# Optimization experiments

Hardware: AMD Instinct MI355X
Metric: run time of the kernel (lower is better)

Reference implementation:

```python
import jax, jax.numpy as jnp
import numpy as np

B, T, EMB, H = 8, 1024, 128, 8


def setup_inputs() -> dict:
    key = jax.random.key(0)
    ks = jax.random.split(key, 7)
    s = 0.02
    return {
        "x": jax.random.normal(ks[0], (B, T, EMB), dtype=jnp.float32),
        "mask": jax.random.randint(ks[1], (1, T, T), 0, 2, dtype=jnp.int32),
        "Wk": (jax.random.normal(ks[2], (EMB * H, EMB), dtype=jnp.float32) * s),
        "Wq": (jax.random.normal(ks[3], (EMB * H, EMB), dtype=jnp.float32) * s),
        "Wv": (jax.random.normal(ks[4], (EMB * H, EMB), dtype=jnp.float32) * s),
        "Wu": (jax.random.normal(ks[5], (EMB, EMB * H), dtype=jnp.float32) * s),
        "bu": (jax.random.normal(ks[6], (EMB,), dtype=jnp.float32) * s),
    }


def reference(x, mask, Wk, Wq, Wv, Wu, bu):
    b, t, e = x.shape  # e == emb; per-head dim also == emb in this module
    h = Wk.shape[0] // e
    # projections: (b,t,e) @ (e, h*e) -> (b,t,h,e) -> (b,h,t,e)
    q = (x @ Wq.T).reshape(b, t, h, e).transpose(0, 2, 1, 3)
    k = (x @ Wk.T).reshape(b, t, h, e).transpose(0, 2, 1, 3)
    v = (x @ Wv.T).reshape(b, t, h, e).transpose(0, 2, 1, 3)
    scale = e ** 0.25  # torch scales q and k each by e**(1/4)
    dot = jnp.einsum('bhqe,bhke->bhqk', q / scale, k / scale)
    # causal mask: strictly-upper triangle (offset=1) set to -inf FIRST
    causal = jnp.triu(jnp.ones((t, t), dtype=bool), k=1)
    dot = jnp.where(causal, -jnp.inf, dot)
    # padding mask: where mask==0 set to -1e9 (overwrites -inf where overlapping)
    dot = jnp.where(mask[:, None] == 0, jnp.float32(-1e9), dot)
    attn = jax.nn.softmax(dot, axis=-1)
    out = jnp.einsum('bhqk,bhke->bhqe', attn, v)
    out = out.transpose(0, 2, 1, 3).reshape(b, t, h * e)
    return out @ Wu.T + bu
```

## Files before the change

kernel.cpp:

```cpp
#include <hip/hip_runtime.h>

#define Bn 8
#define Hn 8
#define Tn 1024
#define Dn 128

typedef __attribute__((ext_vector_type(8))) short bf16x8;
typedef __attribute__((ext_vector_type(4))) float f32x4;

typedef __attribute__((address_space(3))) unsigned int lds_as_t;
typedef __attribute__((address_space(1))) const unsigned int glb_as_t;

static __device__ __forceinline__ void gload_lds16(const unsigned short* g, unsigned short* l) {
    __builtin_amdgcn_global_load_lds((glb_as_t*)g, (lds_as_t*)l, 16, 0, 0);
}
static __device__ __forceinline__ void gload_lds16b(const char* g, char* l) {
    __builtin_amdgcn_global_load_lds((glb_as_t*)g, (lds_as_t*)l, 16, 0, 0);
}

static __device__ __forceinline__ unsigned short f2bf(float f) {
    union { float f; unsigned int u; } v; v.f = f;
    unsigned int u = v.u;
    return (unsigned short)((u + 0x7FFFu + ((u >> 16) & 1u)) >> 16);
}
static __device__ __forceinline__ int pack_bf16_trunc(float lo, float hi) {
    union { float f; unsigned int u; } a, b;
    a.f = lo; b.f = hi;
    return (int)__builtin_amdgcn_perm(b.u, a.u, 0x07060302u);
}

__global__ __launch_bounds__(256) void prep_kernel(
    const float* __restrict__ x,  const float* __restrict__ Wq,
    const float* __restrict__ Wk, const float* __restrict__ Wv,
    const float* __restrict__ Wu, const int* __restrict__ mask,
    unsigned short* __restrict__ xb,  unsigned short* __restrict__ wqB,
    unsigned short* __restrict__ wkB, unsigned short* __restrict__ wvB,
    unsigned short* __restrict__ wuR, unsigned long long* __restrict__ bits)
{
    const int blk = blockIdx.x;
    const int tid = threadIdx.x;

    if (blk < 1408) {
        const float* in; unsigned short* out; int i4;
        if (blk < 1024)      { in = x;  out = xb;  i4 = blk * 256 + tid; }
        else if (blk < 1152) { in = Wq; out = wqB; i4 = (blk - 1024) * 256 + tid; }
        else if (blk < 1280) { in = Wk; out = wkB; i4 = (blk - 1152) * 256 + tid; }
        else                 { in = Wv; out = wvB; i4 = (blk - 1280) * 256 + tid; }
        float4 f = ((const float4*)in)[i4];
        ushort4 o;
        o.x = f2bf(f.x); o.y = f2bf(f.y); o.z = f2bf(f.z); o.w = f2bf(f.w);
        int base = i4 * 4;
        int row = base >> 7, col = base & 127;
        int scol = (((col >> 3) ^ (row & 15)) << 3) | (col & 7);
        *(ushort4*)(out + row * 128 + scol) = o;
    } else if (blk < 1536) {
        int fid = (blk - 1408) * 128 + tid;
        if (tid < 128) {
            int lane_ = fid & 63;
            int l16_ = lane_ & 15, quad_ = lane_ >> 4;
            int nt = (fid >> 6) & 7, kk = fid >> 9;
            int row = nt * 16 + l16_;
            int col = kk * 32 + quad_ * 8;
            const float* src = Wu + (size_t)row * 1024 + col;
            float4 f0 = *(const float4*)(src);
            float4 f1 = *(const float4*)(src + 4);
            unsigned short o[8];
            o[0] = f2bf(f0.x); o[1] = f2bf(f0.y); o[2] = f2bf(f0.z); o[3] = f2bf(f0.w);
            o[4] = f2bf(f1.x); o[5] = f2bf(f1.y); o[6] = f2bf(f1.z); o[7] = f2bf(f1.w);
            *(ushort4*)(wuR + (size_t)fid * 8)     = *(ushort4*)&o[0];
            *(ushort4*)(wuR + (size_t)fid * 8 + 4) = *(ushort4*)&o[4];
        }
    } else {
        int wid  = (blk - 1536) * 4 + (tid >> 6);
        int lane = tid & 63;
#pragma unroll
        for (int i = 0; i < 4; i++) {
            int widx = wid * 4 + i;
            int row = widx >> 4, kt = widx & 15;
            int v = mask[row * Tn + kt * 64 + lane];
            unsigned long long b = __ballot(v != 0);
            if (lane == 0) bits[kt * Tn + row] = b;
        }
    }
}

__global__ __launch_bounds__(256, 2) void qkv_kernel(
    const unsigned short* __restrict__ xb,
    const unsigned short* __restrict__ wqB,
    const unsigned short* __restrict__ wkB,
    const unsigned short* __restrict__ wvB,
    char* __restrict__ Q,
    char* __restrict__ K,
    unsigned short* __restrict__ Vt)
{
    const int bx = blockIdx.x, by = blockIdx.y;
    const int wave = threadIdx.x >> 6;
    const int lane = threadIdx.x & 63;
    const int l16  = lane & 15;
    const int quad = lane >> 4;
    const int wm = wave & 1, wn = wave >> 1;

    __shared__ __align__(16) unsigned short As[128 * 128];
    __shared__ __align__(16) unsigned short Bs[128 * 128];

    const int which = by >> 3;
    const unsigned short* wsel = (which == 0) ? wqB : (which == 1) ? wkB : wvB;
    const unsigned short* Ag = xb + (size_t)bx * 128 * 128;
    const unsigned short* Bg = wsel + (size_t)(by & 7) * 128 * 128;

#pragma unroll
    for (int i = 0; i < 8; i++) {
        int base = (wave * 8 + i) * 512;
        gload_lds16(Ag + base + lane * 8, &As[base]);
        gload_lds16(Bg + base + lane * 8, &Bs[base]);
    }
    __syncthreads();

    bf16x8 a[4][4];
#pragma unroll
    for (int mt = 0; mt < 4; mt++) {
        int row = wm * 64 + mt * 16 + l16;
#pragma unroll
        for (int ks = 0; ks < 4; ks++)
            a[mt][ks] = *(const bf16x8*)(&As[row * 128 + (((ks * 4 + quad) ^ (row & 15)) << 3)]);
    }

    f32x4 acc[4][4];
#pragma unroll
    for (int nt = 0; nt < 4; nt++) {
        int row = wn * 64 + nt * 16 + l16;
        bf16x8 b4[4];
#pragma unroll
        for (int ks = 0; ks < 4; ks++)
            b4[ks] = *(const bf16x8*)(&Bs[row * 128 + (((ks * 4 + quad) ^ (row & 15)) << 3)]);
#pragma unroll
        for (int mt = 0; mt < 4; mt++) {
            f32x4 c = {0.f, 0.f, 0.f, 0.f};
#pragma unroll
            for (int ks = 0; ks < 4; ks++)
                c = __builtin_amdgcn_mfma_f32_16x16x32_bf16(a[mt][ks], b4[ks], c, 0, 0, 0);
            acc[mt][nt] = c;
        }
    }

    const int h_ = by & 7;
    if (which < 2) {
        __syncthreads();
        char* tile = (char*)As;
#pragma unroll
        for (int mt = 0; mt < 4; mt++) {
#pragma unroll
            for (int nt = 0; nt < 4; nt++) {
                int w = __builtin_amdgcn_cvt_pk_fp8_f32(acc[mt][nt][0], acc[mt][nt][1], 0, false);
                w = __builtin_amdgcn_cvt_pk_fp8_f32(acc[mt][nt][2], acc[mt][nt][3], w, true);
                int col = wn * 64 + nt * 16 + l16;
#pragma unroll
                for (int r = 0; r < 4; r++)
                    tile[(wm * 64 + mt * 16 + quad * 4 + r) * 144 + col] = (char)(w >> (8 * r));
            }
        }
        __syncthreads();

        const int f = threadIdx.x;
        int row = f >> 1;
        int t_in = (bx & 7) * 128 + row;
        int b_ = bx >> 3;
        char* dst = (which == 0) ? Q : K;
        size_t rowbase = ((size_t)((b_ * Hn + h_) * Tn + t_in)) * 128;
#pragma unroll
        for (int i = 0; i < 4; i++) {
            int c = (f & 1) * 4 + i;
            int4 v = *(const int4*)(tile + row * 144 + c * 16);
            int cc = (which == 1) ? (c ^ (row & 7)) : c;
            *(int4*)(dst + rowbase + cc * 16) = v;
        }
    } else {
#pragma unroll
        for (int mt = 0; mt < 4; mt++) {
            int m_base = bx * 128 + wm * 64 + mt * 16 + quad * 4;
            int b_ = m_base >> 10;
            int t0 = m_base & 1023;
#pragma unroll
            for (int nt = 0; nt < 4; nt++) {
                int e_ = wn * 64 + nt * 16 + l16;
                int kt_ = t0 >> 6, tc0 = t0 & 63;
                size_t off = ((((size_t)(b_ * Hn + h_) * 16 + kt_) * 128 + e_) << 6)
                           + ((((tc0 >> 3) ^ (e_ & 7)) << 3) | (tc0 & 7));
                ushort4 v4;
                v4.x = f2bf(acc[mt][nt][0]); v4.y = f2bf(acc[mt][nt][1]);
                v4.z = f2bf(acc[mt][nt][2]); v4.w = f2bf(acc[mt][nt][3]);
                *(ushort4*)(Vt + off) = v4;
            }
        }
    }
}

__global__ __launch_bounds__(256, 3) void attn_kernel(
    const char* __restrict__ Q,
    const char* __restrict__ K,
    const unsigned short* __restrict__ Vt,
    const unsigned long long* __restrict__ mbits,
    unsigned short* __restrict__ AO)
{
    const int qt   = 15 - ((blockIdx.x + blockIdx.y) & 15);
    const int bh   = blockIdx.y;
    const int wave = threadIdx.x >> 6;
    const int lane = threadIdx.x & 63;
    const int l16  = lane & 15;
    const int quad = lane >> 4;

    __shared__ __align__(16) char kbuf[2][64 * 128];
    __shared__ __align__(16) unsigned short vbuf[2][128 * 64];

    const char* Qb = Q  + (size_t)bh * Tn * Dn;
    const char* Kb = K  + (size_t)bh * Tn * Dn;
    const unsigned short* Vb = Vt + (size_t)bh * (16 * 128 * 64);

    const int q0 = qt * 64 + wave * 16;
    const int qrow = q0 + quad * 4;

    long qf[4];
#pragma unroll
    for (int ks = 0; ks < 4; ks++)
        qf[ks] = *(const long*)(Qb + (size_t)(q0 + l16) * 128 + ks * 32 + quad * 8);

    bf16x8 ones;
#pragma unroll
    for (int j = 0; j < 8; j++) ones[j] = (short)0x3F80;

    f32x4 o[8];
#pragma unroll
    for (int et = 0; et < 8; et++) o[et] = (f32x4){0.f, 0.f, 0.f, 0.f};
    f32x4 lacc = {0.f, 0.f, 0.f, 0.f};

    const float SL = 0.12752041570284543f;

    const int idx0 = (l16 << 2) + ((quad & 1) << 7);
    const int idx1 = idx0 + 64;
    const bool hiQ = (quad >> 1) != 0;

#pragma unroll
    for (int i = 0; i < 2; i++) {
        int base = (wave * 2 + i) * 1024;
        gload_lds16b(Kb + base + lane * 16, &kbuf[0][base]);
    }
#pragma unroll
    for (int i = 0; i < 4; i++) {
        int base = (wave * 4 + i) * 512;
        gload_lds16(Vb + base + lane * 8, &vbuf[0][base]);
    }

    for (int kt = 0; kt <= qt; kt++) {
        const int cur = kt & 1;
        __syncthreads();

        if (kt < qt) {
            const char* Kg = Kb + (kt + 1) * (64 * 128);
            const unsigned short* Vg = Vb + (kt + 1) * (128 * 64);
#pragma unroll
            for (int i = 0; i < 2; i++) {
                int base = (wave * 2 + i) * 1024;
                gload_lds16b(Kg + base + lane * 16, &kbuf[cur ^ 1][base]);
            }
#pragma unroll
            for (int i = 0; i < 4; i++) {
                int base = (wave * 4 + i) * 512;
                gload_lds16(Vg + base + lane * 8, &vbuf[cur ^ 1][base]);
            }
        }

        const unsigned long long mw = mbits[kt * Tn + q0 + l16];

        f32x4 s[4];
#pragma unroll
        for (int nt = 0; nt < 4; nt++) {
            int row = nt * 16 + l16;
            long a4[4];
#pragma unroll
            for (int ks = 0; ks < 4; ks++) {
                int c = ks * 2 + (quad >> 1);
                a4[ks] = *(const long*)(&kbuf[cur][row * 128 + (((c ^ (row & 7)) << 4) | ((quad & 1) << 3))]);
            }
            f32x4 c = {0.f, 0.f, 0.f, 0.f};
#pragma unroll
            for (int ks = 0; ks < 4; ks++)
                c = __builtin_amdgcn_mfma_f32_16x16x32_fp8_fp8(a4[ks], qf[ks], c, 0, 0, 0);
            s[nt] = c;
        }

        const int kc0 = kt * 64;
        const int qglob = q0 + l16;
        int w[4][2];
#pragma unroll
        for (int nt = 0; nt < 4; nt++) {
            float pv[4];
#pragma unroll
            for (int r = 0; r < 4; r++) {
                int bit = nt * 16 + quad * 4 + r;
                bool live = ((mw >> bit) & 1ULL) && (kc0 + bit <= qglob);
                pv[r] = live ? __builtin_amdgcn_exp2f(s[nt][r] * SL) : 0.f;
            }
            w[nt][0] = pack_bf16_trunc(pv[0], pv[1]);
            w[nt][1] = pack_bf16_trunc(pv[2], pv[3]);
        }

        bf16x8 pf[2];
#pragma unroll
        for (int k2 = 0; k2 < 2; k2++) {
            union { int i[4]; bf16x8 v; } u;
#pragma unroll
            for (int d = 0; d < 4; d++) {
                int idx = (d < 2) ? idx0 : idx1;
                int va = __builtin_amdgcn_ds_bpermute(idx, w[2 * k2][d & 1]);
                int vb = __builtin_amdgcn_ds_bpermute(idx, w[2 * k2 + 1][d & 1]);
                u.i[d] = hiQ ? vb : va;
            }
            pf[k2] = u.v;
        }

#pragma unroll
        for (int k2 = 0; k2 < 2; k2++)
            lacc = __builtin_amdgcn_mfma_f32_16x16x32_bf16(pf[k2], ones, lacc, 0, 0, 0);

#pragma unroll
        for (int et = 0; et < 8; et++) {
            int row = et * 16 + l16;
#pragma unroll
            for (int k2 = 0; k2 < 2; k2++) {
                bf16x8 b = *(const bf16x8*)(&vbuf[cur][row * 64 + (((k2 * 4 + quad) ^ (l16 & 7)) << 3)]);
                o[et] = __builtin_amdgcn_mfma_f32_16x16x32_bf16(pf[k2], b, o[et], 0, 0, 0);
            }
        }
    }

    __syncthreads();
    {
        bool deg = (lacc[0] == 0.f) | (lacc[1] == 0.f) | (lacc[2] == 0.f) | (lacc[3] == 0.f);
        if (__ballot(deg) != 0ULL) {
            unsigned short* pb = (unsigned short*)((char*)kbuf + wave * 2304);
            unsigned short dsel[4];
#pragma unroll
            for (int r = 0; r < 4; r++) dsel[r] = (lacc[r] == 0.f) ? (unsigned short)0x3F80 : (unsigned short)0;
            for (int kt = 0; kt < 16; kt++) {
                unsigned long long mw2[4];
#pragma unroll
                for (int r = 0; r < 4; r++) mw2[r] = mbits[kt * Tn + qrow + r];
#pragma unroll
                for (int nt = 0; nt < 4; nt++) {
                    int bi = nt * 16 + l16;
#pragma unroll
                    for (int r = 0; r < 4; r++)
                        pb[(quad * 4 + r) * 72 + bi] = ((mw2[r] >> bi) & 1ULL) ? (unsigned short)0 : dsel[r];
                }
                bf16x8 pf[2];
#pragma unroll
                for (int k2 = 0; k2 < 2; k2++)
                    pf[k2] = *(const bf16x8*)(&pb[l16 * 72 + k2 * 32 + quad * 8]);
#pragma unroll
                for (int k2 = 0; k2 < 2; k2++)
                    lacc = __builtin_amdgcn_mfma_f32_16x16x32_bf16(pf[k2], ones, lacc, 0, 0, 0);
                const unsigned short* Vg = Vb + kt * (128 * 64);
#pragma unroll
                for (int et = 0; et < 8; et++) {
#pragma unroll
                    for (int k2 = 0; k2 < 2; k2++) {
                        bf16x8 b = *(const bf16x8*)(Vg + (et * 16 + l16) * 64 + (((k2 * 4 + quad) ^ (l16 & 7)) << 3));
                        o[et] = __builtin_amdgcn_mfma_f32_16x16x32_bf16(pf[k2], b, o[et], 0, 0, 0);
                    }
                }
            }
        }
    }

    const int b_ = bh >> 3, h_ = bh & 7;
#pragma unroll
    for (int r = 0; r < 4; r++) {
        float inv = 1.f / lacc[r];
        int q = qrow + r;
        size_t rowoff = (size_t)(b_ * Tn + q) * (Hn * Dn) + h_ * Dn;
#pragma unroll
        for (int et = 0; et < 8; et++)
            AO[rowoff + et * 16 + l16] = f2bf(o[et][r] * inv);
    }
}

__global__ __launch_bounds__(256) void outproj_kernel(
    const unsigned short* __restrict__ AO,
    const unsigned short* __restrict__ wuR,
    const float* __restrict__ bu,
    float* __restrict__ out)
{
    const int wave = threadIdx.x >> 6;
    const int lane = threadIdx.x & 63;
    const int l16  = lane & 15;
    const int quad = lane >> 4;
    const int m0 = blockIdx.x * 16;

    __shared__ float red[4][16][128];

    f32x4 acc[8];
#pragma unroll
    for (int nt = 0; nt < 8; nt++) acc[nt] = (f32x4){0.f, 0.f, 0.f, 0.f};

    const int kk0 = wave * 8;
#pragma unroll
    for (int g = 0; g < 8; g++) {
        int kk = kk0 + g;
        bf16x8 a = *(const bf16x8*)(AO + (size_t)(m0 + l16) * 1024 + kk * 32 + quad * 8);
#pragma unroll
        for (int nt = 0; nt < 8; nt++) {
            bf16x8 b = *(const bf16x8*)(wuR + ((size_t)(kk * 8 + nt) * 64 + lane) * 8);
            acc[nt] = __builtin_amdgcn_mfma_f32_16x16x32_bf16(a, b, acc[nt], 0, 0, 0);
        }
    }

#pragma unroll
    for (int nt = 0; nt < 8; nt++)
#pragma unroll
        for (int r = 0; r < 4; r++)
            red[wave][quad * 4 + r][nt * 16 + l16] = acc[nt][r];
    __syncthreads();

#pragma unroll
    for (int i = 0; i < 2; i++) {
        int flat = threadIdx.x * 2 + i;
        int row = flat >> 5, c4 = (flat & 31) * 4;
        f32x4 v = *(const f32x4*)(&red[0][row][c4]);
#pragma unroll
        for (int w = 1; w < 4; w++) {
            f32x4 p = *(const f32x4*)(&red[w][row][c4]);
            v[0] += p[0]; v[1] += p[1]; v[2] += p[2]; v[3] += p[3];
        }
        float4 bb = *(const float4*)(bu + c4);
        v[0] += bb.x; v[1] += bb.y; v[2] += bb.z; v[3] += bb.w;
        *(f32x4*)(out + (size_t)(m0 + row) * Dn + c4) = v;
    }
}

extern "C" void kernel_launch(void* const* d_in, const int* in_sizes, int n_in,
                              void* d_out, int out_size, void* d_ws, size_t ws_size,
                              hipStream_t stream) {
    const float* x   = (const float*)d_in[0];
    const int* mask  = (const int*)d_in[1];
    const float* Wk  = (const float*)d_in[2];
    const float* Wq  = (const float*)d_in[3];
    const float* Wv  = (const float*)d_in[4];
    const float* Wu  = (const float*)d_in[5];
    const float* bu  = (const float*)d_in[6];
    float* out = (float*)d_out;

    char* ws = (char*)d_ws;
    unsigned short* xb  = (unsigned short*)ws; ws += (size_t)8192 * 128 * 2;
    unsigned short* wqB = (unsigned short*)ws; ws += (size_t)1024 * 128 * 2;
    unsigned short* wkB = (unsigned short*)ws; ws += (size_t)1024 * 128 * 2;
    unsigned short* wvB = (unsigned short*)ws; ws += (size_t)1024 * 128 * 2;
    unsigned short* wuR = (unsigned short*)ws; ws += (size_t)128 * 1024 * 2;
    char* Qf  = ws; ws += (size_t)64 * 1024 * 128;
    char* Kf  = ws; ws += (size_t)64 * 1024 * 128;
    unsigned short* Vtw = (unsigned short*)ws; ws += (size_t)64 * 1024 * 128 * 2;
    unsigned short* AOw = (unsigned short*)ws; ws += (size_t)8192 * 1024 * 2;
    unsigned long long* mb = (unsigned long long*)ws; ws += (size_t)1024 * 16 * 8;

    prep_kernel<<<dim3(2560), 256, 0, stream>>>(x, Wq, Wk, Wv, Wu, mask,
                                                xb, wqB, wkB, wvB, wuR, mb);
    qkv_kernel<<<dim3(64, 24), 256, 0, stream>>>(xb, wqB, wkB, wvB, Qf, Kf, Vtw);
    attn_kernel<<<dim3(16, 64), 256, 0, stream>>>(Qf, Kf, Vtw, mb, AOw);
    outproj_kernel<<<dim3(512), 256, 0, stream>>>(AOw, wuR, bu, out);
}
```

Before: 149.3 us.

## Fuse output projection into attention epilogue with per-head atomic accumulation

Removes the separate output-projection kernel and the bf16 AO intermediate buffer. Each attention wave normalizes its 16x128 head output, stages it through LDS, multiplies it by that head's slice of Wu with MFMA, and atomically adds the result into the fp32 output. The prep kernel now pre-fills the output with the bias and reorders Wu per head. This saves the AO write/read round trip and one launch, at the cost of 8-way fp32 atomics per output element, extra register pressure in the attention kernel, and a summation order that is no longer deterministic.

```diff
diff --git a/kernel.cpp b/kernel.cpp
--- a/kernel.cpp
+++ b/kernel.cpp
@@ -33,9 +33,10 @@
     const float* __restrict__ x,  const float* __restrict__ Wq,
     const float* __restrict__ Wk, const float* __restrict__ Wv,
     const float* __restrict__ Wu, const int* __restrict__ mask,
+    const float* __restrict__ bu, float* __restrict__ outp,
     unsigned short* __restrict__ xb,  unsigned short* __restrict__ wqB,
     unsigned short* __restrict__ wkB, unsigned short* __restrict__ wvB,
-    unsigned short* __restrict__ wuR, unsigned long long* __restrict__ bits)
+    unsigned short* __restrict__ wuF, unsigned long long* __restrict__ bits)
 {
     const int blk = blockIdx.x;
     const int tid = threadIdx.x;
@@ -54,23 +55,23 @@
         int scol = (((col >> 3) ^ (row & 15)) << 3) | (col & 7);
         *(ushort4*)(out + row * 128 + scol) = o;
     } else if (blk < 1536) {
-        int fid = (blk - 1408) * 128 + tid;
         if (tid < 128) {
-            int lane_ = fid & 63;
-            int l16_ = lane_ & 15, quad_ = lane_ >> 4;
-            int nt = (fid >> 6) & 7, kk = fid >> 9;
-            int row = nt * 16 + l16_;
-            int col = kk * 32 + quad_ * 8;
+            int id = (blk - 1408) * 128 + tid;
+            int lane_ = id & 63;
+            int fid = id >> 6;
+            int nt = fid & 7, ks = (fid >> 3) & 3, h = fid >> 5;
+            int row = nt * 16 + (lane_ & 15);
+            int col = h * 128 + ks * 32 + (lane_ >> 4) * 8;
             const float* src = Wu + (size_t)row * 1024 + col;
             float4 f0 = *(const float4*)(src);
             float4 f1 = *(const float4*)(src + 4);
             unsigned short o[8];
             o[0] = f2bf(f0.x); o[1] = f2bf(f0.y); o[2] = f2bf(f0.z); o[3] = f2bf(f0.w);
             o[4] = f2bf(f1.x); o[5] = f2bf(f1.y); o[6] = f2bf(f1.z); o[7] = f2bf(f1.w);
-            *(ushort4*)(wuR + (size_t)fid * 8)     = *(ushort4*)&o[0];
-            *(ushort4*)(wuR + (size_t)fid * 8 + 4) = *(ushort4*)&o[4];
-        }
-    } else {
+            *(ushort4*)(wuF + (size_t)id * 8)     = *(ushort4*)&o[0];
+            *(ushort4*)(wuF + (size_t)id * 8 + 4) = *(ushort4*)&o[4];
+        }
+    } else if (blk < 2560) {
         int wid  = (blk - 1536) * 4 + (tid >> 6);
         int lane = tid & 63;
 #pragma unroll
@@ -81,6 +82,11 @@
             unsigned long long b = __ballot(v != 0);
             if (lane == 0) bits[kt * Tn + row] = b;
         }
+    } else {
+        int f4 = (blk - 2560) * 1024 + tid * 4;
+#pragma unroll
+        for (int i = 0; i < 4; i++)
+            ((float4*)outp)[f4 + i] = ((const float4*)bu)[(f4 + i) & 31];
     }
 }
 
@@ -200,7 +206,8 @@
     const char* __restrict__ K,
     const unsigned short* __restrict__ Vt,
     const unsigned long long* __restrict__ mbits,
-    unsigned short* __restrict__ AO)
+    const unsigned short* __restrict__ wuF,
+    float* __restrict__ out)
 {
     const int qt   = 15 - ((blockIdx.x + blockIdx.y) & 15);
     const int bh   = blockIdx.y;
@@ -373,67 +380,44 @@
     }
 
     const int b_ = bh >> 3, h_ = bh & 7;
-#pragma unroll
-    for (int r = 0; r < 4; r++) {
-        float inv = 1.f / lacc[r];
-        int q = qrow + r;
-        size_t rowoff = (size_t)(b_ * Tn + q) * (Hn * Dn) + h_ * Dn;
-#pragma unroll
-        for (int et = 0; et < 8; et++)
-            AO[rowoff + et * 16 + l16] = f2bf(o[et][r] * inv);
-    }
-}
-
-__global__ __launch_bounds__(256) void outproj_kernel(
-    const unsigned short* __restrict__ AO,
-    const unsigned short* __restrict__ wuR,
-    const float* __restrict__ bu,
-    float* __restrict__ out)
-{
-    const int wave = threadIdx.x >> 6;
-    const int lane = threadIdx.x & 63;
-    const int l16  = lane & 15;
-    const int quad = lane >> 4;
-    const int m0 = blockIdx.x * 16;
-
-    __shared__ float red[4][16][128];
-
-    f32x4 acc[8];
-#pragma unroll
-    for (int nt = 0; nt < 8; nt++) acc[nt] = (f32x4){0.f, 0.f, 0.f, 0.f};
-
-    const int kk0 = wave * 8;
-#pragma unroll
-    for (int g = 0; g < 8; g++) {
-        int kk = kk0 + g;
-        bf16x8 a = *(const bf16x8*)(AO + (size_t)(m0 + l16) * 1024 + kk * 32 + quad * 8);
+    {
+        unsigned short* tile = (unsigned short*)((char*)vbuf + wave * 4608);
+#pragma unroll
+        for (int r = 0; r < 4; r++) {
+            float inv = 1.f / lacc[r];
+            int row = quad * 4 + r;
+#pragma unroll
+            for (int et = 0; et < 8; et++)
+                tile[row * 144 + et * 16 + l16] = f2bf(o[et][r] * inv);
+        }
+
+        bf16x8 a4[4];
+#pragma unroll
+        for (int ks = 0; ks < 4; ks++)
+            a4[ks] = *(const bf16x8*)(&tile[l16 * 144 + ks * 32 + quad * 8]);
+
+        const unsigned short* wf = wuF + (size_t)h_ * (4 * 8 * 64 * 8);
+        f32x4 acc2[8];
+#pragma unroll
+        for (int nt = 0; nt < 8; nt++) acc2[nt] = (f32x4){0.f, 0.f, 0.f, 0.f};
+#pragma unroll
+        for (int ks = 0; ks < 4; ks++) {
+#pragma unroll
+            for (int nt = 0; nt < 8; nt++) {
+                bf16x8 b = *(const bf16x8*)(wf + ((size_t)(ks * 8 + nt) * 64 + lane) * 8);
+                acc2[nt] = __builtin_amdgcn_mfma_f32_16x16x32_bf16(a4[ks], b, acc2[nt], 0, 0, 0);
+            }
+        }
+
 #pragma unroll
         for (int nt = 0; nt < 8; nt++) {
-            bf16x8 b = *(const bf16x8*)(wuR + ((size_t)(kk * 8 + nt) * 64 + lane) * 8);
-            acc[nt] = __builtin_amdgcn_mfma_f32_16x16x32_bf16(a, b, acc[nt], 0, 0, 0);
-        }
-    }
-
-#pragma unroll
-    for (int nt = 0; nt < 8; nt++)
-#pragma unroll
-        for (int r = 0; r < 4; r++)
-            red[wave][quad * 4 + r][nt * 16 + l16] = acc[nt][r];
-    __syncthreads();
-
-#pragma unroll
-    for (int i = 0; i < 2; i++) {
-        int flat = threadIdx.x * 2 + i;
-        int row = flat >> 5, c4 = (flat & 31) * 4;
-        f32x4 v = *(const f32x4*)(&red[0][row][c4]);
-#pragma unroll
-        for (int w = 1; w < 4; w++) {
-            f32x4 p = *(const f32x4*)(&red[w][row][c4]);
-            v[0] += p[0]; v[1] += p[1]; v[2] += p[2]; v[3] += p[3];
-        }
-        float4 bb = *(const float4*)(bu + c4);
-        v[0] += bb.x; v[1] += bb.y; v[2] += bb.z; v[3] += bb.w;
-        *(f32x4*)(out + (size_t)(m0 + row) * Dn + c4) = v;
+            int n = nt * 16 + l16;
+#pragma unroll
+            for (int r = 0; r < 4; r++) {
+                int q = q0 + quad * 4 + r;
+                atomicAdd(&out[(size_t)(b_ * Tn + q) * Dn + n], acc2[nt][r]);
+            }
+        }
     }
 }
 
@@ -454,16 +438,14 @@
     unsigned short* wqB = (unsigned short*)ws; ws += (size_t)1024 * 128 * 2;
     unsigned short* wkB = (unsigned short*)ws; ws += (size_t)1024 * 128 * 2;
     unsigned short* wvB = (unsigned short*)ws; ws += (size_t)1024 * 128 * 2;
-    unsigned short* wuR = (unsigned short*)ws; ws += (size_t)128 * 1024 * 2;
+    unsigned short* wuF = (unsigned short*)ws; ws += (size_t)128 * 1024 * 2;
     char* Qf  = ws; ws += (size_t)64 * 1024 * 128;
     char* Kf  = ws; ws += (size_t)64 * 1024 * 128;
     unsigned short* Vtw = (unsigned short*)ws; ws += (size_t)64 * 1024 * 128 * 2;
-    unsigned short* AOw = (unsigned short*)ws; ws += (size_t)8192 * 1024 * 2;
     unsigned long long* mb = (unsigned long long*)ws; ws += (size_t)1024 * 16 * 8;
 
-    prep_kernel<<<dim3(2560), 256, 0, stream>>>(x, Wq, Wk, Wv, Wu, mask,
-                                                xb, wqB, wkB, wvB, wuR, mb);
+    prep_kernel<<<dim3(2816), 256, 0, stream>>>(x, Wq, Wk, Wv, Wu, mask, bu, out,
+                                                xb, wqB, wkB, wvB, wuF, mb);
     qkv_kernel<<<dim3(64, 24), 256, 0, stream>>>(xb, wqB, wkB, wvB, Qf, Kf, Vtw);
-    attn_kernel<<<dim3(16, 64), 256, 0, stream>>>(Qf, Kf, Vtw, mb, AOw);
-    outproj_kernel<<<dim3(512), 256, 0, stream>>>(AOw, wuR, bu, out);
-}
+    attn_kernel<<<dim3(16, 64), 256, 0, stream>>>(Qf, Kf, Vtw, mb, wuF, out);
+}
```

New measurement: 147.9 us. No clear change (-1.0%).
